# Kernel tuning notes

Hardware: AMD Instinct MI355X
Metric: run time of the kernel (lower is better)

Reference implementation:

```python
import jax, jax.numpy as jnp
import numpy as np

B, N, FEAT_DIM = 64, 4096, 256
N_SLOTS, SLOT_DIM, N_ITERS = 6, 64, 3
EPS_LN = 1e-5

def _ln(x, g, b):
    m = jnp.mean(x, axis=-1, keepdims=True)
    v = jnp.mean((x - m) ** 2, axis=-1, keepdims=True)
    return (x - m) * jax.lax.rsqrt(v + EPS_LN) * g + b

def setup_inputs() -> dict:
    key = jax.random.key(0)
    ks = jax.random.split(key, 16)
    def lin(k, out_d, in_d):  # torch Linear default init scale
        bound = 1.0 / np.sqrt(in_d)
        return jax.random.uniform(k, (out_d, in_d), jnp.float32, -bound, bound)
    H = SLOT_DIM
    bound_h = 1.0 / np.sqrt(H)
    return {
        "features": jax.random.normal(ks[0], (B, N, FEAT_DIM), jnp.float32),
        "slot_noise": jax.random.normal(ks[1], (B, N_SLOTS, SLOT_DIM), jnp.float32),
        "slot_mu": jax.random.normal(ks[2], (1, 1, SLOT_DIM), jnp.float32) * 0.02,
        "slot_sigma": jnp.ones((1, 1, SLOT_DIM), jnp.float32) * 0.1,
        "ln_feat_g": jnp.ones((FEAT_DIM,), jnp.float32),
        "ln_feat_b": jnp.zeros((FEAT_DIM,), jnp.float32),
        "ln_slot_g": jnp.ones((SLOT_DIM,), jnp.float32),
        "ln_slot_b": jnp.zeros((SLOT_DIM,), jnp.float32),
        "ln_mlp_g": jnp.ones((SLOT_DIM,), jnp.float32),
        "ln_mlp_b": jnp.zeros((SLOT_DIM,), jnp.float32),
        "Wk": lin(ks[3], SLOT_DIM, FEAT_DIM),
        "Wv": lin(ks[4], SLOT_DIM, FEAT_DIM),
        "Wq": lin(ks[5], SLOT_DIM, SLOT_DIM),
        "W_ih": jax.random.uniform(ks[6], (3 * H, H), jnp.float32, -bound_h, bound_h),
        "W_hh": jax.random.uniform(ks[7], (3 * H, H), jnp.float32, -bound_h, bound_h),
        "b_ih": jax.random.uniform(ks[8], (3 * H,), jnp.float32, -bound_h, bound_h),
        "b_hh": jax.random.uniform(ks[9], (3 * H,), jnp.float32, -bound_h, bound_h),
        "mlp_W1": lin(ks[10], 2 * SLOT_DIM, SLOT_DIM),
        "mlp_b1": jnp.zeros((2 * SLOT_DIM,), jnp.float32),
        "mlp_W2": lin(ks[11], SLOT_DIM, 2 * SLOT_DIM),
        "mlp_b2": jnp.zeros((SLOT_DIM,), jnp.float32),
    }

def _gru(x, h, W_ih, W_hh, b_ih, b_hh):
    # torch.nn.GRUCell semantics; x, h: [M, H]
    gi = x @ W_ih.T + b_ih
    gh = h @ W_hh.T + b_hh
    i_r, i_z, i_n = jnp.split(gi, 3, axis=-1)
    h_r, h_z, h_n = jnp.split(gh, 3, axis=-1)
    r = jax.nn.sigmoid(i_r + h_r)
    z = jax.nn.sigmoid(i_z + h_z)
    n = jnp.tanh(i_n + r * h_n)
    return (1.0 - z) * n + z * h

def reference(features, slot_noise, slot_mu, slot_sigma,
              ln_feat_g, ln_feat_b, ln_slot_g, ln_slot_b, ln_mlp_g, ln_mlp_b,
              Wk, Wv, Wq, W_ih, W_hh, b_ih, b_hh,
              mlp_W1, mlp_b1, mlp_W2, mlp_b2):
    slots = slot_mu + slot_sigma * slot_noise            # [B, K, H]
    f = _ln(features, ln_feat_g, ln_feat_b)              # [B, N, D]
    k = jnp.einsum('bnd,hd->bnh', f, Wk)                 # [B, N, H]
    v = jnp.einsum('bnd,hd->bnh', f, Wv)                 # [B, N, H]
    scale = SLOT_DIM ** (-0.5)
    for _ in range(N_ITERS):
        slots_prev = slots
        s = _ln(slots, ln_slot_g, ln_slot_b)
        q = jnp.einsum('bkh,gh->bkg', s, Wq)             # [B, K, H]
        attn = jnp.einsum('bkh,bnh->bkn', q, k) * scale  # [B, K, N]
        attn = jax.nn.softmax(attn, axis=1)              # softmax over SLOT dim
        attn = attn / (jnp.sum(attn, axis=-1, keepdims=True) + 1e-8)
        updates = jnp.einsum('bkn,bnh->bkh', attn, v)    # [B, K, H]
        h = _gru(updates.reshape(-1, SLOT_DIM), slots_prev.reshape(-1, SLOT_DIM),
                 W_ih, W_hh, b_ih, b_hh)
        slots = h.reshape(B, N_SLOTS, SLOT_DIM)
        m = _ln(slots, ln_mlp_g, ln_mlp_b)
        m = jax.nn.relu(m @ mlp_W1.T + mlp_b1) @ mlp_W2.T + mlp_b2
        slots = slots + m
    return slots
```

## Files before the change

### kernel.cpp

```cpp
#include <hip/hip_runtime.h>
#include <hip/hip_bf16.h>
#include <math.h>

#define B_SZ    64
#define N_TOK   4096
#define D_FEAT  256
#define K_SLOTS 6
#define H_DIM   64
#define N_IT    3
#define CHUNKS  16
#define ATTN_TILES ((N_TOK / CHUNKS) / 64)
#define LNKV_BLOCKS 512
#define TILES_PER_BLOCK 8

typedef __attribute__((ext_vector_type(8))) __bf16 bf16x8;
typedef __attribute__((ext_vector_type(4))) __bf16 bf16x4;
typedef __attribute__((ext_vector_type(4))) float  f32x4v;

__device__ __forceinline__ float wave_reduce_sum(float v) {
    #pragma unroll
    for (int off = 32; off > 0; off >>= 1) v += __shfl_xor(v, off, 64);
    return v;
}
__device__ __forceinline__ float bflo(unsigned u) { return __builtin_bit_cast(float, (unsigned)(u << 16)); }
__device__ __forceinline__ float bfhi(unsigned u) { return __builtin_bit_cast(float, (unsigned)(u & 0xffff0000u)); }

__global__ __launch_bounds__(256) void prep_kernel(
    const float* __restrict__ Wk, const float* __restrict__ Wv,
    const float* __restrict__ noise, const float* __restrict__ mu,
    const float* __restrict__ sigma, const float* __restrict__ Wq,
    const float* __restrict__ W_ih, const float* __restrict__ W_hh,
    const float* __restrict__ W1, const float* __restrict__ W2,
    __bf16* __restrict__ Wfrag, float* __restrict__ slots,
    float* __restrict__ WqT, float* __restrict__ WihT, float* __restrict__ WhhT,
    float* __restrict__ W1T, float* __restrict__ W2T)
{
    const int tg = blockIdx.x * 256 + threadIdx.x;
    if (tg < 4096) {
        const int chunk = tg >> 6, lane = tg & 63;
        const int ct = chunk >> 3, ks = chunk & 7;
        const int outr = ct * 16 + (lane & 15);
        const int dbase = (lane >> 4) * 8 + ks * 32;
        const float* srcw = (outr < 64) ? &Wk[outr * 256] : &Wv[(outr - 64) * 256];
        bf16x8 w8;
        #pragma unroll
        for (int j = 0; j < 8; ++j) w8[j] = (__bf16)srcw[dbase + j];
        *(bf16x8*)&Wfrag[(size_t)tg * 8] = w8;
    } else if (tg < 4096 + 24576) {
        const int i = tg - 4096;
        const int hh = i & 63;
        slots[i] = mu[hh] + sigma[hh] * noise[i];
    } else if (tg < 32768) {
        const int i = tg - 28672;
        WqT[i] = Wq[(i & 63) * 64 + (i >> 6)];
    } else if (tg < 45056) {
        const int i = tg - 32768;
        WihT[i] = W_ih[(i % 192) * 64 + (i / 192)];
    } else if (tg < 57344) {
        const int i = tg - 45056;
        WhhT[i] = W_hh[(i % 192) * 64 + (i / 192)];
    } else if (tg < 65536) {
        const int i = tg - 57344;
        W1T[i] = W1[(i & 127) * 64 + (i >> 7)];
    } else if (tg < 73728) {
        const int i = tg - 65536;
        W2T[i] = W2[(i & 63) * 128 + (i >> 6)];
    }
}

__global__ __launch_bounds__(256, 2) void ln_kv_mfma(
    const float* __restrict__ feat, const float* __restrict__ g,
    const float* __restrict__ bta, const __bf16* __restrict__ Wfrag,
    __bf16* __restrict__ kv)
{
    __shared__ __align__(16) __bf16 A_lds[64][264];
    __shared__ __align__(16) __bf16 C_lds[64][136];

    const int t = threadIdx.x;
    const int lane = t & 63;
    const int w = t >> 6;
    const int m15 = lane & 15;
    const int q4 = lane >> 4;

    bf16x8 wf[2][8];
    #pragma unroll
    for (int c2 = 0; c2 < 2; ++c2)
        #pragma unroll
        for (int ks = 0; ks < 8; ++ks)
            wf[c2][ks] = *(const bf16x8*)&Wfrag[(size_t)(((2 * w + c2) * 8 + ks) * 64 + lane) * 8];

    const float4 gg = *(const float4*)&g[lane * 4];
    const float4 bb = *(const float4*)&bta[lane * 4];

    float4 x[16];
    {
        const size_t row0 = (size_t)blockIdx.x * TILES_PER_BLOCK * 64 + w * 16;
        #pragma unroll
        for (int r = 0; r < 16; ++r)
            x[r] = *(const float4*)&feat[(row0 + r) * D_FEAT + lane * 4];
    }

    for (int tile = 0; tile < TILES_PER_BLOCK; ++tile) {
        const size_t tile_row0 = (size_t)blockIdx.x * TILES_PER_BLOCK * 64 + (size_t)tile * 64;

        float s1[16], s2[16];
        #pragma unroll
        for (int r = 0; r < 16; ++r) {
            s1[r] = x[r].x + x[r].y + x[r].z + x[r].w;
            s2[r] = x[r].x * x[r].x + x[r].y * x[r].y + x[r].z * x[r].z + x[r].w * x[r].w;
        }
        #pragma unroll
        for (int off = 32; off > 0; off >>= 1) {
            #pragma unroll
            for (int r = 0; r < 16; ++r) {
                s1[r] += __shfl_xor(s1[r], off, 64);
                s2[r] += __shfl_xor(s2[r], off, 64);
            }
        }
        #pragma unroll
        for (int r = 0; r < 16; ++r) {
            const float m = s1[r] * (1.0f / 256.0f);
            const float inv = rsqrtf(s2[r] * (1.0f / 256.0f) - m * m + 1e-5f);
            bf16x4 y;
            y[0] = (__bf16)((x[r].x - m) * inv * gg.x + bb.x);
            y[1] = (__bf16)((x[r].y - m) * inv * gg.y + bb.y);
            y[2] = (__bf16)((x[r].z - m) * inv * gg.z + bb.z);
            y[3] = (__bf16)((x[r].w - m) * inv * gg.w + bb.w);
            *(bf16x4*)&A_lds[w * 16 + r][lane * 4] = y;
        }

        if (tile + 1 < TILES_PER_BLOCK) {
            const size_t row0 = tile_row0 + 64 + w * 16;
            #pragma unroll
            for (int r = 0; r < 16; ++r)
                x[r] = *(const float4*)&feat[(row0 + r) * D_FEAT + lane * 4];
        }

        __syncthreads();

        f32x4v acc[4][2];
        #pragma unroll
        for (int mt = 0; mt < 4; ++mt) {
            acc[mt][0] = (f32x4v){0.f, 0.f, 0.f, 0.f};
            acc[mt][1] = (f32x4v){0.f, 0.f, 0.f, 0.f};
        }
        #pragma unroll
        for (int ks = 0; ks < 8; ++ks) {
            #pragma unroll
            for (int mt = 0; mt < 4; ++mt) {
                const bf16x8 af = *(const bf16x8*)&A_lds[mt * 16 + m15][q4 * 8 + ks * 32];
                acc[mt][0] = __builtin_amdgcn_mfma_f32_16x16x32_bf16(af, wf[0][ks], acc[mt][0], 0, 0, 0);
                acc[mt][1] = __builtin_amdgcn_mfma_f32_16x16x32_bf16(af, wf[1][ks], acc[mt][1], 0, 0, 0);
            }
        }

        #pragma unroll
        for (int mt = 0; mt < 4; ++mt)
            #pragma unroll
            for (int c2 = 0; c2 < 2; ++c2)
                #pragma unroll
                for (int reg = 0; reg < 4; ++reg)
                    C_lds[mt * 16 + q4 * 4 + reg][(2 * w + c2) * 16 + m15] = (__bf16)acc[mt][c2][reg];

        __syncthreads();

        const int lr = w * 16 + (lane >> 2);
        const int seg = lane & 3;
        __bf16* dstg = kv + (tile_row0 + lr) * 128 + seg * 32;
        #pragma unroll
        for (int u = 0; u < 4; ++u) {
            const uint4 val = *(const uint4*)&C_lds[lr][seg * 32 + u * 8];
            *(uint4*)&dstg[u * 8] = val;
        }
    }
}

__global__ __launch_bounds__(64) void slot_q0(
    const float* __restrict__ slots, const float* __restrict__ g,
    const float* __restrict__ bta, const float* __restrict__ WqT,
    float* __restrict__ qb)
{
    __shared__ float s_lds[64];
    const int bk = blockIdx.x, h = threadIdx.x;
    const float xv = slots[bk * 64 + h];
    const float s1 = wave_reduce_sum(xv);
    const float s2 = wave_reduce_sum(xv * xv);
    const float m = s1 * (1.0f / 64.0f);
    const float inv = rsqrtf(s2 * (1.0f / 64.0f) - m * m + 1e-5f);
    s_lds[h] = (xv - m) * inv * g[h] + bta[h];
    __syncthreads();
    float acc = 0.f;
    #pragma unroll 8
    for (int j = 0; j < 64; ++j) acc += WqT[j * 64 + h] * s_lds[j];
    qb[bk * 64 + h] = acc;
}

__global__ __launch_bounds__(256, 4) void attn_kernel(
    const float* __restrict__ qb, const __bf16* __restrict__ kv,
    float* __restrict__ U_part, float* __restrict__ S_part)
{
    __shared__ float q_lds[K_SLOTS * 64];
    __shared__ __align__(16) __bf16 Vt[64][64];
    __shared__ float p_lds[K_SLOTS][64];
    __shared__ float U_red[4][K_SLOTS][64];
    __shared__ float S_red[4][K_SLOTS];

    const int t = threadIdx.x;
    const int b = blockIdx.y;
    const int chunk = blockIdx.x;
    const int lane = t & 63;
    const int w = t >> 6;
    const int n_loc = t >> 2, sub = t & 3;
    const int h = lane;

    for (int i = t; i < K_SLOTS * 64; i += 256) q_lds[i] = qb[b * K_SLOTS * 64 + i] * 0.125f;

    float Uacc[K_SLOTS] = {0, 0, 0, 0, 0, 0};
    float Sacc[K_SLOTS] = {0, 0, 0, 0, 0, 0};

    const size_t chunk_base = (size_t)b * N_TOK + (size_t)chunk * (N_TOK / CHUNKS);

    uint4 k0, k1, v0, v1;
    {
        const uint4* ksrc = (const uint4*)&kv[(chunk_base + n_loc) * 128 + sub * 16];
        k0 = ksrc[0]; k1 = ksrc[1];
        const uint4* vsrc = (const uint4*)&kv[(chunk_base + (t >> 2)) * 128 + 64 + (t & 3) * 16];
        v0 = vsrc[0]; v1 = vsrc[1];
    }

    for (int tile = 0; tile < ATTN_TILES; ++tile) {
        __syncthreads();

        *(uint4*)&Vt[t >> 2][(t & 3) * 16] = v0;
        *(uint4*)&Vt[t >> 2][(t & 3) * 16 + 8] = v1;

        float kf[16];
        kf[0]  = bflo(k0.x); kf[1]  = bfhi(k0.x); kf[2]  = bflo(k0.y); kf[3]  = bfhi(k0.y);
        kf[4]  = bflo(k0.z); kf[5]  = bfhi(k0.z); kf[6]  = bflo(k0.w); kf[7]  = bfhi(k0.w);
        kf[8]  = bflo(k1.x); kf[9]  = bfhi(k1.x); kf[10] = bflo(k1.y); kf[11] = bfhi(k1.y);
        kf[12] = bflo(k1.z); kf[13] = bfhi(k1.z); kf[14] = bflo(k1.w); kf[15] = bfhi(k1.w);

        uint4 nk0, nk1, nv0, nv1;
        if (tile + 1 < ATTN_TILES) {
            const size_t n0n = chunk_base + (size_t)(tile + 1) * 64;
            const uint4* ksrc = (const uint4*)&kv[(n0n + n_loc) * 128 + sub * 16];
            nk0 = ksrc[0]; nk1 = ksrc[1];
            const uint4* vsrc = (const uint4*)&kv[(n0n + (t >> 2)) * 128 + 64 + (t & 3) * 16];
            nv0 = vsrc[0]; nv1 = vsrc[1];
        }

        float part[K_SLOTS];
        #pragma unroll
        for (int k = 0; k < K_SLOTS; ++k) {
            const float4* q4p = (const float4*)&q_lds[k * 64 + sub * 16];
            const float4 qa = q4p[0], qb4 = q4p[1], qc = q4p[2], qd = q4p[3];
            part[k] = qa.x * kf[0]  + qa.y * kf[1]  + qa.z * kf[2]  + qa.w * kf[3]
                    + qb4.x * kf[4] + qb4.y * kf[5] + qb4.z * kf[6] + qb4.w * kf[7]
                    + qc.x * kf[8]  + qc.y * kf[9]  + qc.z * kf[10] + qc.w * kf[11]
                    + qd.x * kf[12] + qd.y * kf[13] + qd.z * kf[14] + qd.w * kf[15];
        }

        #pragma unroll
        for (int k = 0; k < K_SLOTS; ++k) {
            part[k] += __shfl_xor(part[k], 1, 64);
            part[k] += __shfl_xor(part[k], 2, 64);
        }
        float mx = part[0];
        #pragma unroll
        for (int k = 1; k < K_SLOTS; ++k) mx = fmaxf(mx, part[k]);
        float e[K_SLOTS], ssum = 0.f;
        #pragma unroll
        for (int k = 0; k < K_SLOTS; ++k) { e[k] = __expf(part[k] - mx); ssum += e[k]; }
        const float rs = 1.0f / ssum;
        if (sub == 0) {
            #pragma unroll
            for (int k = 0; k < K_SLOTS; ++k) {
                const float p = e[k] * rs;
                p_lds[k][n_loc] = p;
                Sacc[k] += p;
            }
        }
        __syncthreads();

        float vf[16];
        #pragma unroll
        for (int i = 0; i < 16; ++i) vf[i] = (float)Vt[w * 16 + i][h];
        #pragma unroll
        for (int k = 0; k < K_SLOTS; ++k) {
            const float4* pp = (const float4*)&p_lds[k][w * 16];
            const float4 p0 = pp[0], p1 = pp[1], p2 = pp[2], p3 = pp[3];
            Uacc[k] += p0.x * vf[0]  + p0.y * vf[1]  + p0.z * vf[2]  + p0.w * vf[3]
                     + p1.x * vf[4]  + p1.y * vf[5]  + p1.z * vf[6]  + p1.w * vf[7]
                     + p2.x * vf[8]  + p2.y * vf[9]  + p2.z * vf[10] + p2.w * vf[11]
                     + p3.x * vf[12] + p3.y * vf[13] + p3.z * vf[14] + p3.w * vf[15];
        }

        k0 = nk0; k1 = nk1; v0 = nv0; v1 = nv1;
    }

    #pragma unroll
    for (int k = 0; k < K_SLOTS; ++k) U_red[w][k][h] = Uacc[k];
    #pragma unroll
    for (int k = 0; k < K_SLOTS; ++k) {
        const float s = wave_reduce_sum(Sacc[k]);
        if (lane == 0) S_red[w][k] = s;
    }
    __syncthreads();
    for (int idx = t; idx < K_SLOTS * 64; idx += 256) {
        const int k = idx >> 6, hh = idx & 63;
        const float s = U_red[0][k][hh] + U_red[1][k][hh] + U_red[2][k][hh] + U_red[3][k][hh];
        U_part[(((size_t)b * CHUNKS + chunk) * K_SLOTS + k) * 64 + hh] = s;
    }
    if (t < K_SLOTS) {
        const float s = S_red[0][t] + S_red[1][t] + S_red[2][t] + S_red[3][t];
        S_part[((size_t)b * CHUNKS + chunk) * K_SLOTS + t] = s;
    }
}

__global__ __launch_bounds__(64) void update_kernel(
    const float* __restrict__ U_part, const float* __restrict__ S_part,
    float* __restrict__ slots,
    const float* __restrict__ WihT, const float* __restrict__ WhhT,
    const float* __restrict__ b_ih, const float* __restrict__ b_hh,
    const float* __restrict__ g_mlp, const float* __restrict__ b_mlp,
    const float* __restrict__ W1T, const float* __restrict__ b1,
    const float* __restrict__ W2T, const float* __restrict__ b2,
    const float* __restrict__ g_slot, const float* __restrict__ b_slot,
    const float* __restrict__ WqT, float* __restrict__ qb,
    float* __restrict__ out, int last)
{
    __shared__ float x_lds[64], h_lds[64], m_lds[64], r_lds[128];
    const int bk = blockIdx.x, h = threadIdx.x;
    const int b = bk / K_SLOTS, k = bk % K_SLOTS;

    float Us = 0.f, Ss = 0.f;
    #pragma unroll
    for (int c = 0; c < CHUNKS; ++c)
        Us += U_part[(((size_t)b * CHUNKS + c) * K_SLOTS + k) * 64 + h];
    #pragma unroll
    for (int c = 0; c < CHUNKS; ++c)
        Ss += S_part[((size_t)b * CHUNKS + c) * K_SLOTS + k];

    const float u = Us / (Ss + 1e-8f);
    const float hp = slots[bk * 64 + h];
    x_lds[h] = u;
    h_lds[h] = hp;
    __syncthreads();

    float ir = b_ih[h], iz = b_ih[64 + h], inn = b_ih[128 + h];
    float hr = b_hh[h], hz = b_hh[64 + h], hn = b_hh[128 + h];
    #pragma unroll 4
    for (int j = 0; j < 64; ++j) {
        const float xj = x_lds[j], hj = h_lds[j];
        const float* wi = &WihT[j * 192];
        const float* wh = &WhhT[j * 192];
        ir += wi[h] * xj; iz += wi[64 + h] * xj; inn += wi[128 + h] * xj;
        hr += wh[h] * hj; hz += wh[64 + h] * hj; hn += wh[128 + h] * hj;
    }
    const float r = 1.0f / (1.0f + __expf(-(ir + hr)));
    const float z = 1.0f / (1.0f + __expf(-(iz + hz)));
    const float nn = tanhf(inn + r * hn);
    const float hnew = (1.0f - z) * nn + z * hp;

    const float s1 = wave_reduce_sum(hnew);
    const float s2 = wave_reduce_sum(hnew * hnew);
    const float m = s1 * (1.0f / 64.0f);
    const float inv = rsqrtf(s2 * (1.0f / 64.0f) - m * m + 1e-5f);
    m_lds[h] = (hnew - m) * inv * g_mlp[h] + b_mlp[h];
    __syncthreads();

    float a1 = b1[h], a2 = b1[64 + h];
    #pragma unroll 4
    for (int j = 0; j < 64; ++j) {
        const float mj = m_lds[j];
        a1 += W1T[j * 128 + h] * mj;
        a2 += W1T[j * 128 + 64 + h] * mj;
    }
    r_lds[h] = fmaxf(a1, 0.f);
    r_lds[64 + h] = fmaxf(a2, 0.f);
    __syncthreads();

    float o = b2[h];
    #pragma unroll 4
    for (int c = 0; c < 128; ++c) o += W2T[c * 64 + h] * r_lds[c];

    const float res = hnew + o;
    slots[bk * 64 + h] = res;
    if (last) {
        out[bk * 64 + h] = res;
    } else {
        const float t1 = wave_reduce_sum(res);
        const float t2 = wave_reduce_sum(res * res);
        const float mm = t1 * (1.0f / 64.0f);
        const float ii = rsqrtf(t2 * (1.0f / 64.0f) - mm * mm + 1e-5f);
        m_lds[h] = (res - mm) * ii * g_slot[h] + b_slot[h];
        __syncthreads();
        float qv = 0.f;
        #pragma unroll 8
        for (int j = 0; j < 64; ++j) qv += WqT[j * 64 + h] * m_lds[j];
        qb[bk * 64 + h] = qv;
    }
}

extern "C" void kernel_launch(void* const* d_in, const int* in_sizes, int n_in,
                              void* d_out, int out_size, void* d_ws, size_t ws_size,
                              hipStream_t stream) {
    const float* feat      = (const float*)d_in[0];
    const float* noise     = (const float*)d_in[1];
    const float* mu        = (const float*)d_in[2];
    const float* sigma     = (const float*)d_in[3];
    const float* ln_feat_g = (const float*)d_in[4];
    const float* ln_feat_b = (const float*)d_in[5];
    const float* ln_slot_g = (const float*)d_in[6];
    const float* ln_slot_b = (const float*)d_in[7];
    const float* ln_mlp_g  = (const float*)d_in[8];
    const float* ln_mlp_b  = (const float*)d_in[9];
    const float* Wk        = (const float*)d_in[10];
    const float* Wv        = (const float*)d_in[11];
    const float* Wq        = (const float*)d_in[12];
    const float* W_ih      = (const float*)d_in[13];
    const float* W_hh      = (const float*)d_in[14];
    const float* b_ih      = (const float*)d_in[15];
    const float* b_hh      = (const float*)d_in[16];
    const float* W1        = (const float*)d_in[17];
    const float* b1        = (const float*)d_in[18];
    const float* W2        = (const float*)d_in[19];
    const float* b2        = (const float*)d_in[20];
    float* out = (float*)d_out;

    char* p = (char*)d_ws;
    __bf16* kv    = (__bf16*)p;                 p += (size_t)B_SZ * N_TOK * 128 * 2;
    __bf16* Wfrag = (__bf16*)p;                 p += 32768 * 2;
    float* slots  = (float*)p;                  p += 24576 * 4;
    float* qb     = (float*)p;                  p += 24576 * 4;
    float* U_part = (float*)p;                  p += (size_t)B_SZ * CHUNKS * K_SLOTS * 64 * 4;
    float* S_part = (float*)p;                  p += (size_t)B_SZ * CHUNKS * K_SLOTS * 4;
    float* WqT    = (float*)p;                  p += 4096 * 4;
    float* WihT   = (float*)p;                  p += 12288 * 4;
    float* WhhT   = (float*)p;                  p += 12288 * 4;
    float* W1T    = (float*)p;                  p += 8192 * 4;
    float* W2T    = (float*)p;                  p += 8192 * 4;

    hipLaunchKernelGGL(prep_kernel, dim3(288), dim3(256), 0, stream,
                       Wk, Wv, noise, mu, sigma, Wq, W_ih, W_hh, W1, W2,
                       Wfrag, slots, WqT, WihT, WhhT, W1T, W2T);
    hipLaunchKernelGGL(ln_kv_mfma, dim3(LNKV_BLOCKS), dim3(256), 0, stream,
                       feat, ln_feat_g, ln_feat_b, Wfrag, kv);
    hipLaunchKernelGGL(slot_q0, dim3(384), dim3(64), 0, stream,
                       slots, ln_slot_g, ln_slot_b, WqT, qb);
    for (int it = 0; it < N_IT; ++it) {
        hipLaunchKernelGGL(attn_kernel, dim3(CHUNKS, B_SZ), dim3(256), 0, stream,
                           qb, kv, U_part, S_part);
        hipLaunchKernelGGL(update_kernel, dim3(384), dim3(64), 0, stream,
                           U_part, S_part, slots, WihT, WhhT, b_ih, b_hh,
                           ln_mlp_g, ln_mlp_b, W1T, b1, W2T, b2,
                           ln_slot_g, ln_slot_b, WqT, qb,
                           out, (it == N_IT - 1) ? 1 : 0);
    }
}
```

Before: 551.1 us.

## Split update kernel matvecs across four waves with LDS reduction

The per-slot GRU/MLP/query update kernel now runs 256 threads per block instead of 64. Each wave handles a quarter of the reduction dimension, broadcasts inputs via wave shuffles instead of LDS, and the partial sums are combined through shared memory. This shortens the serial dependent matvec chains in a latency-bound small kernel, at the cost of extra LDS traffic, barriers and redundant per-wave work.

After: 502.0 us. -8.9%, faster.

```diff
diff --git a/kernel.cpp b/kernel.cpp
--- a/kernel.cpp
+++ b/kernel.cpp
@@ -317,7 +317,7 @@
     }
 }
 
-__global__ __launch_bounds__(64) void update_kernel(
+__global__ __launch_bounds__(256) void update_kernel(
     const float* __restrict__ U_part, const float* __restrict__ S_part,
     float* __restrict__ slots,
     const float* __restrict__ WihT, const float* __restrict__ WhhT,
@@ -329,33 +329,47 @@
     const float* __restrict__ WqT, float* __restrict__ qb,
     float* __restrict__ out, int last)
 {
-    __shared__ float x_lds[64], h_lds[64], m_lds[64], r_lds[128];
-    const int bk = blockIdx.x, h = threadIdx.x;
+    __shared__ float g_red[4][6][64];
+    __shared__ float m_red[4][2][64];
+    __shared__ float o_red[4][64];
+    __shared__ float q_red[4][64];
+
+    const int t = threadIdx.x;
+    const int lane = t & 63;
+    const int w = t >> 6;
+    const int bk = blockIdx.x;
     const int b = bk / K_SLOTS, k = bk % K_SLOTS;
 
     float Us = 0.f, Ss = 0.f;
     #pragma unroll
-    for (int c = 0; c < CHUNKS; ++c)
-        Us += U_part[(((size_t)b * CHUNKS + c) * K_SLOTS + k) * 64 + h];
-    #pragma unroll
-    for (int c = 0; c < CHUNKS; ++c)
+    for (int c = 0; c < CHUNKS; ++c) {
+        Us += U_part[(((size_t)b * CHUNKS + c) * K_SLOTS + k) * 64 + lane];
         Ss += S_part[((size_t)b * CHUNKS + c) * K_SLOTS + k];
-
+    }
     const float u = Us / (Ss + 1e-8f);
-    const float hp = slots[bk * 64 + h];
-    x_lds[h] = u;
-    h_lds[h] = hp;
-    __syncthreads();
-
-    float ir = b_ih[h], iz = b_ih[64 + h], inn = b_ih[128 + h];
-    float hr = b_hh[h], hz = b_hh[64 + h], hn = b_hh[128 + h];
-    #pragma unroll 4
-    for (int j = 0; j < 64; ++j) {
-        const float xj = x_lds[j], hj = h_lds[j];
+    const float hp = slots[bk * 64 + lane];
+
+    float pr0 = 0.f, pr1 = 0.f, pr2 = 0.f, pr3 = 0.f, pr4 = 0.f, pr5 = 0.f;
+    #pragma unroll
+    for (int jj = 0; jj < 16; ++jj) {
+        const int j = w * 16 + jj;
+        const float xj = __shfl(u, j, 64);
+        const float hj = __shfl(hp, j, 64);
         const float* wi = &WihT[j * 192];
         const float* wh = &WhhT[j * 192];
-        ir += wi[h] * xj; iz += wi[64 + h] * xj; inn += wi[128 + h] * xj;
-        hr += wh[h] * hj; hz += wh[64 + h] * hj; hn += wh[128 + h] * hj;
+        pr0 += wi[lane] * xj; pr1 += wi[64 + lane] * xj; pr2 += wi[128 + lane] * xj;
+        pr3 += wh[lane] * hj; pr4 += wh[64 + lane] * hj; pr5 += wh[128 + lane] * hj;
+    }
+    g_red[w][0][lane] = pr0; g_red[w][1][lane] = pr1; g_red[w][2][lane] = pr2;
+    g_red[w][3][lane] = pr3; g_red[w][4][lane] = pr4; g_red[w][5][lane] = pr5;
+    __syncthreads();
+
+    float ir = b_ih[lane], iz = b_ih[64 + lane], inn = b_ih[128 + lane];
+    float hr = b_hh[lane], hz = b_hh[64 + lane], hn = b_hh[128 + lane];
+    #pragma unroll
+    for (int ww = 0; ww < 4; ++ww) {
+        ir += g_red[ww][0][lane]; iz += g_red[ww][1][lane]; inn += g_red[ww][2][lane];
+        hr += g_red[ww][3][lane]; hz += g_red[ww][4][lane]; hn += g_red[ww][5][lane];
     }
     const float r = 1.0f / (1.0f + __expf(-(ir + hr)));
     const float z = 1.0f / (1.0f + __expf(-(iz + hz)));
@@ -366,39 +380,61 @@
     const float s2 = wave_reduce_sum(hnew * hnew);
     const float m = s1 * (1.0f / 64.0f);
     const float inv = rsqrtf(s2 * (1.0f / 64.0f) - m * m + 1e-5f);
-    m_lds[h] = (hnew - m) * inv * g_mlp[h] + b_mlp[h];
+    const float mv = (hnew - m) * inv * g_mlp[lane] + b_mlp[lane];
+
+    float a1 = 0.f, a2 = 0.f;
+    #pragma unroll
+    for (int jj = 0; jj < 16; ++jj) {
+        const int j = w * 16 + jj;
+        const float mj = __shfl(mv, j, 64);
+        a1 += W1T[j * 128 + lane] * mj;
+        a2 += W1T[j * 128 + 64 + lane] * mj;
+    }
+    m_red[w][0][lane] = a1; m_red[w][1][lane] = a2;
     __syncthreads();
 
-    float a1 = b1[h], a2 = b1[64 + h];
-    #pragma unroll 4
-    for (int j = 0; j < 64; ++j) {
-        const float mj = m_lds[j];
-        a1 += W1T[j * 128 + h] * mj;
-        a2 += W1T[j * 128 + 64 + h] * mj;
-    }
-    r_lds[h] = fmaxf(a1, 0.f);
-    r_lds[64 + h] = fmaxf(a2, 0.f);
+    float f1 = b1[lane], f2 = b1[64 + lane];
+    #pragma unroll
+    for (int ww = 0; ww < 4; ++ww) { f1 += m_red[ww][0][lane]; f2 += m_red[ww][1][lane]; }
+    const float r1 = fmaxf(f1, 0.f), r2 = fmaxf(f2, 0.f);
+
+    float op = 0.f;
+    #pragma unroll
+    for (int cc = 0; cc < 32; ++cc) {
+        const int c = w * 32 + cc;
+        const float rc = (c < 64) ? __shfl(r1, c, 64) : __shfl(r2, c - 64, 64);
+        op += W2T[c * 64 + lane] * rc;
+    }
+    o_red[w][lane] = op;
     __syncthreads();
 
-    float o = b2[h];
-    #pragma unroll 4
-    for (int c = 0; c < 128; ++c) o += W2T[c * 64 + h] * r_lds[c];
-
+    float o = b2[lane];
+    #pragma unroll
+    for (int ww = 0; ww < 4; ++ww) o += o_red[ww][lane];
     const float res = hnew + o;
-    slots[bk * 64 + h] = res;
-    if (last) {
-        out[bk * 64 + h] = res;
-    } else {
+
+    if (w == 0) {
+        slots[bk * 64 + lane] = res;
+        if (last) out[bk * 64 + lane] = res;
+    }
+
+    if (!last) {
         const float t1 = wave_reduce_sum(res);
         const float t2 = wave_reduce_sum(res * res);
         const float mm = t1 * (1.0f / 64.0f);
         const float ii = rsqrtf(t2 * (1.0f / 64.0f) - mm * mm + 1e-5f);
-        m_lds[h] = (res - mm) * ii * g_slot[h] + b_slot[h];
+        const float mq = (res - mm) * ii * g_slot[lane] + b_slot[lane];
+        float qp = 0.f;
+        #pragma unroll
+        for (int jj = 0; jj < 16; ++jj) {
+            const int j = w * 16 + jj;
+            qp += WqT[j * 64 + lane] * __shfl(mq, j, 64);
+        }
+        q_red[w][lane] = qp;
         __syncthreads();
-        float qv = 0.f;
-        #pragma unroll 8
-        for (int j = 0; j < 64; ++j) qv += WqT[j * 64 + h] * m_lds[j];
-        qb[bk * 64 + h] = qv;
+        if (w == 0) {
+            qb[bk * 64 + lane] = q_red[0][lane] + q_red[1][lane] + q_red[2][lane] + q_red[3][lane];
+        }
     }
 }
 
@@ -451,7 +487,7 @@
     for (int it = 0; it < N_IT; ++it) {
         hipLaunchKernelGGL(attn_kernel, dim3(CHUNKS, B_SZ), dim3(256), 0, stream,
                            qb, kv, U_part, S_part);
-        hipLaunchKernelGGL(update_kernel, dim3(384), dim3(64), 0, stream,
+        hipLaunchKernelGGL(update_kernel, dim3(384), dim3(256), 0, stream,
                            U_part, S_part, slots, WihT, WhhT, b_ih, b_hh,
                            ln_mlp_g, ln_mlp_b, W1T, b1, W2T, b2,
                            ln_slot_g, ln_slot_b, WqT, qb,
```
